# Optimization experiments

Measured on AMD Instinct MI355X. Metric: run time of the kernel, lower is better.

Reference implementation:

```python
import jax, jax.numpy as jnp
import numpy as np

EPS = 1e-7  # tf.keras.backend.epsilon()
DEGREE = 5
SCALE_BASE = 1.0
SCALE_LEGENDRE = 1.0


def legendre_basis(x, degree):
    # min/max normalization over the feature axis -> x_norm in [-1, 1]
    x_min = jnp.min(x, axis=-1, keepdims=True)
    x_max = jnp.max(x, axis=-1, keepdims=True)
    x_norm = 2.0 * (x - x_min) / (x_max - x_min + EPS) - 1.0
    polys = [jnp.ones_like(x_norm), x_norm]
    for n in range(2, degree + 1):
        p_n = ((2 * n - 1) * x_norm * polys[-1] - (n - 1) * polys[-2]) / n
        polys.append(p_n)
    return jnp.stack(polys, axis=-1)  # [b, i, degree+1]


def setup_inputs() -> dict:
    key = jax.random.key(0)
    k1, k2, k3 = jax.random.split(key, 3)
    b, i, o, d = 4096, 1024, 1024, DEGREE + 1
    x = jax.random.normal(k1, (b, i), dtype=jnp.float32)
    # HeUniform: limit = sqrt(6 / fan_in)
    lim_b = np.sqrt(6.0 / i)
    base_weight = jax.random.uniform(k2, (i, o), dtype=jnp.float32, minval=-lim_b, maxval=lim_b)
    legendre_weight = jax.random.uniform(k3, (i, o, d), dtype=jnp.float32, minval=-lim_b, maxval=lim_b)
    return {"x": x, "base_weight": base_weight, "legendre_weight": legendre_weight}


def reference(x, base_weight, legendre_weight):
    base_output = jax.nn.silu(x @ base_weight)  # [b, o]
    basis = legendre_basis(x, DEGREE)  # [b, i, d]
    # 'bi,iod,bid->bo' == fold x into the basis then contract (i, d)
    xb = x[..., None] * basis  # [b, i, d]
    legendre_output = jnp.einsum('bid,iod->bo', xb, legendre_weight)
    return SCALE_BASE * base_output + SCALE_LEGENDRE * legendre_output
```

## Files before the change

### kernel.cpp

```cpp
#include <hip/hip_runtime.h>
#include <stdint.h>

typedef unsigned short u16;
typedef unsigned int   u32;
typedef __attribute__((ext_vector_type(8))) short bhalf8;
typedef __attribute__((ext_vector_type(4))) float f32x4;

#define B_ROWS 4096
#define I_DIM  1024
#define O_DIM  1024
#define N_D    6
#define K_LEG  (I_DIM * N_D)

#define BM 256
#define BN 256
#define BK 32
#define NU 56
#define SLOT_BYTES 32768
#define LDS_BYTES  131072

__device__ __forceinline__ u16 f2b(float f) {
  u32 u = __float_as_uint(f);
  return (u16)((u + 0x7fffu + ((u >> 16) & 1u)) >> 16);
}

__device__ __forceinline__ void gld_lds16(const void* g, void* l) {
  __builtin_amdgcn_global_load_lds(
      (const __attribute__((address_space(1))) u32*)(uintptr_t)g,
      (__attribute__((address_space(3))) u32*)(u32)(uintptr_t)l, 16, 0, 0);
}

#define RS 201
__global__ void k_prep_w(const float* __restrict__ bw, const float* __restrict__ lw,
                         u16* __restrict__ Bb, u16* __restrict__ Bl) {
  __shared__ float t[32 * RS];
  if (blockIdx.x < 1024) {
    const int bx = blockIdx.x & 31, by = blockIdx.x >> 5;
    const int i0 = by * 32, o0 = bx * 32;
    const int c = threadIdx.x & 31, r0 = threadIdx.x >> 5;
    #pragma unroll
    for (int k = 0; k < 4; ++k) {
      int r = r0 + k * 8;
      t[r * 33 + c] = bw[(size_t)(i0 + r) * O_DIM + o0 + c];
    }
    __syncthreads();
    #pragma unroll
    for (int k = 0; k < 4; ++k) {
      int r = r0 + k * 8;
      Bb[(size_t)(o0 + r) * I_DIM + i0 + c] = f2b(t[c * 33 + r]);
    }
  } else {
    const int blk = blockIdx.x - 1024;
    const int bx = blk & 31, by = blk >> 5;
    const int i0 = by * 32, o0 = bx * 32;
    for (int q = threadIdx.x; q < 32 * 48; q += 256) {
      int ri = q / 48, s4 = q % 48;
      float4 v = *(const float4*)(lw + (size_t)(i0 + ri) * (O_DIM * N_D) + o0 * N_D + s4 * 4);
      float* p = t + ri * RS + s4 * 4;
      p[0] = v.x; p[1] = v.y; p[2] = v.z; p[3] = v.w;
    }
    __syncthreads();
    for (int q = threadIdx.x; q < 32 * 96; q += 256) {
      int ro = q / 96, k = q % 96;
      int e0 = 2 * k, e1 = 2 * k + 1;
      float v0 = t[(e0 / 6) * RS + ro * 6 + (e0 % 6)];
      float v1 = t[(e1 / 6) * RS + ro * 6 + (e1 % 6)];
      u32* dst = (u32*)(Bl + (size_t)(o0 + ro) * K_LEG + i0 * N_D);
      dst[k] = (u32)f2b(v0) | ((u32)f2b(v1) << 16);
    }
  }
}

__global__ void k_prep_basis(const float* __restrict__ x,
                             u16* __restrict__ Ab, u16* __restrict__ Al) {
  int b = blockIdx.x;
  int t = threadIdx.x;
  float4 v = ((const float4*)(x + (size_t)b * I_DIM))[t];
  float mn = fminf(fminf(v.x, v.y), fminf(v.z, v.w));
  float mx = fmaxf(fmaxf(v.x, v.y), fmaxf(v.z, v.w));
  #pragma unroll
  for (int off = 32; off > 0; off >>= 1) {
    mn = fminf(mn, __shfl_xor(mn, off, 64));
    mx = fmaxf(mx, __shfl_xor(mx, off, 64));
  }
  __shared__ float smn[4], smx[4];
  if ((t & 63) == 0) { smn[t >> 6] = mn; smx[t >> 6] = mx; }
  __syncthreads();
  mn = fminf(fminf(smn[0], smn[1]), fminf(smn[2], smn[3]));
  mx = fmaxf(fmaxf(smx[0], smx[1]), fmaxf(smx[2], smx[3]));
  float sc = 2.0f / (mx - mn + 1e-7f);

  float xs[4] = {v.x, v.y, v.z, v.w};
  u32 lb[12];
  #pragma unroll
  for (int e = 0; e < 4; ++e) {
    float xv = xs[e];
    float xn = (xv - mn) * sc - 1.0f;
    float p0 = 1.0f, p1 = xn;
    float p2 = (3.0f * xn * p1 - 1.0f * p0) * (1.0f / 2.0f);
    float p3 = (5.0f * xn * p2 - 2.0f * p1) * (1.0f / 3.0f);
    float p4 = (7.0f * xn * p3 - 3.0f * p2) * (1.0f / 4.0f);
    float p5 = (9.0f * xn * p4 - 4.0f * p3) * (1.0f / 5.0f);
    lb[e * 3 + 0] = (u32)f2b(xv * p0) | ((u32)f2b(xv * p1) << 16);
    lb[e * 3 + 1] = (u32)f2b(xv * p2) | ((u32)f2b(xv * p3) << 16);
    lb[e * 3 + 2] = (u32)f2b(xv * p4) | ((u32)f2b(xv * p5) << 16);
  }
  u32 a0 = (u32)f2b(xs[0]) | ((u32)f2b(xs[1]) << 16);
  u32 a1 = (u32)f2b(xs[2]) | ((u32)f2b(xs[3]) << 16);
  *(uint2*)(Ab + (size_t)b * I_DIM + t * 4) = make_uint2(a0, a1);
  uint4* dl = (uint4*)(Al + (size_t)b * K_LEG + t * 24);
  dl[0] = make_uint4(lb[0], lb[1], lb[2], lb[3]);
  dl[1] = make_uint4(lb[4], lb[5], lb[6], lb[7]);
  dl[2] = make_uint4(lb[8], lb[9], lb[10], lb[11]);
}

__global__ __launch_bounds__(512, 2) void k_gemm(
    const u16* __restrict__ Ab, const u16* __restrict__ Bb,
    const u16* __restrict__ Al, const u16* __restrict__ Bl,
    float* __restrict__ out, float* __restrict__ P) {
  extern __shared__ char lds[];

  const int tid  = threadIdx.x;
  const int wave = tid >> 6;
  const int lane = tid & 63;
  const int wm = wave >> 2;
  const int wn = wave & 3;
  const int rr = lane & 15;
  const int kg = lane >> 4;

  const int bid   = blockIdx.x;
  const int bx    = bid >> 4;
  const int by    = (bid >> 2) & 3;
  const int split = bid & 3;
  const size_t brow = (size_t)bx * BM;
  const size_t bcol = (size_t)by * BN;
  const bool s0 = (split == 0);
  const int legbase = s0 ? 0 : (24 + 56 * (split - 1));

  const int r4 = tid >> 2;
  const size_t cs = (size_t)((((tid & 3) ^ ((r4 >> 1) & 3))) * 8);
  char* const l0 = lds + (u32)wave * 1024;

  const u16 *gA0, *gA1, *gB0, *gB1;
  auto set_ptrs = [&](const u16* A, const u16* Bt, size_t ldk, size_t kt) {
    const size_t ko = kt * BK + cs;
    gA0 = A  + (brow + r4) * ldk + ko;
    gA1 = A  + (brow + 128 + r4) * ldk + ko;
    gB0 = Bt + (bcol + r4) * ldk + ko;
    gB1 = Bt + (bcol + 128 + r4) * ldk + ko;
  };
  if (s0) set_ptrs(Ab, Bb, I_DIM, 0);
  else    set_ptrs(Al, Bl, K_LEG, (size_t)legbase);

  const u32 axor  = (u32)((kg ^ ((rr >> 1) & 3)) * 16);
  const u32 abase = (u32)((wm * 128 + rr) * 64) + axor;
  const u32 bbase = 16384u + (u32)((wn * 64 + rr) * 64) + axor;

  f32x4 acc[8][4] = {};
  bhalf8 af_[4], af2_[4], bf_[4];

  #pragma unroll
  for (int v = 0; v < 3; ++v) {
    char* d = l0 + (size_t)v * SLOT_BYTES;
    gld_lds16(gA0, d);          gld_lds16(gA1, d + 8192);
    gld_lds16(gB0, d + 16384);  gld_lds16(gB1, d + 24576);
    gA0 += BK; gA1 += BK; gB0 += BK; gB1 += BK;
  }
  asm volatile("s_waitcnt vmcnt(8)" ::: "memory");
  __builtin_amdgcn_s_barrier();

#define PH0(u, DO_STAGE) do {                                                 \
    const char* p_ = lds + (size_t)((u) & 3) * SLOT_BYTES;                    \
    _Pragma("unroll")                                                         \
    for (int n = 0; n < 4; ++n) bf_[n] = *(const bhalf8*)(p_ + bbase + n * 1024); \
    _Pragma("unroll")                                                         \
    for (int m = 0; m < 4; ++m) af_[m] = *(const bhalf8*)(p_ + abase + m * 1024); \
    if (DO_STAGE) {                                                           \
      char* d_ = l0 + (size_t)(((u) + 3) & 3) * SLOT_BYTES;                   \
      gld_lds16(gA0, d_); gld_lds16(gA1, d_ + 8192);                          \
    }                                                                         \
    asm volatile("" ::: "memory");                                            \
    __builtin_amdgcn_s_barrier();                                             \
    asm volatile("s_waitcnt lgkmcnt(0)" ::: "memory");                        \
    __builtin_amdgcn_s_setprio(1);                                            \
    _Pragma("unroll")                                                         \
    for (int m = 0; m < 4; ++m)                                               \
      _Pragma("unroll")                                                       \
      for (int n = 0; n < 4; ++n)                                             \
        acc[m][n] = __builtin_amdgcn_mfma_f32_16x16x32_bf16(af_[m], bf_[n], acc[m][n], 0, 0, 0); \
    __builtin_amdgcn_s_setprio(0);                                            \
    __builtin_amdgcn_s_barrier();                                             \
  } while (0)

#define PH1(u, DO_STAGE, VM) do {                                             \
    const char* p_ = lds + (size_t)((u) & 3) * SLOT_BYTES;                    \
    _Pragma("unroll")                                                         \
    for (int m = 0; m < 4; ++m) af2_[m] = *(const bhalf8*)(p_ + abase + (4 + m) * 1024); \
    if (DO_STAGE) {                                                           \
      char* d_ = l0 + (size_t)(((u) + 3) & 3) * SLOT_BYTES;                   \
      gld_lds16(gB0, d_ + 16384); gld_lds16(gB1, d_ + 24576);                 \
      if (s0 && (u) + 4 == 32) set_ptrs(Al, Bl, K_LEG, 0);                    \
      else { gA0 += BK; gA1 += BK; gB0 += BK; gB1 += BK; }                    \
    }                                                                         \
    asm volatile("s_waitcnt vmcnt(" #VM ")" ::: "memory");                    \
    __builtin_amdgcn_s_barrier();                                             \
    asm volatile("s_waitcnt lgkmcnt(0)" ::: "memory");                        \
    __builtin_amdgcn_s_setprio(1);                                            \
    _Pragma("unroll")                                                         \
    for (int m = 0; m < 4; ++m)                                               \
      _Pragma("unroll")                                                       \
      for (int n = 0; n < 4; ++n)                                             \
        acc[4 + m][n] = __builtin_amdgcn_mfma_f32_16x16x32_bf16(af2_[m], bf_[n], acc[4 + m][n], 0, 0, 0); \
    __builtin_amdgcn_s_setprio(0);                                            \
    __builtin_amdgcn_s_barrier();                                             \
  } while (0)

  for (int u = 0; u < NU - 3; ++u) {
    if (s0 && u == 32) {
      #pragma unroll
      for (int m = 0; m < 8; ++m)
        #pragma unroll
        for (int n = 0; n < 4; ++n)
          #pragma unroll
          for (int j = 0; j < 4; ++j) {
            float v = acc[m][n][j];
            acc[m][n][j] = v / (1.0f + __expf(-v));
          }
    }
    PH0(u, true);
    PH1(u, true, 8);
  }
  PH0(53, false); PH1(53, false, 4);
  PH0(54, false); PH1(54, false, 0);
  PH0(55, false); PH1(55, false, 0);
#undef PH0
#undef PH1

  float* dst = s0 ? out : (P + (size_t)(split - 1) * ((size_t)B_ROWS * O_DIM));
  #pragma unroll
  for (int m = 0; m < 8; ++m)
    #pragma unroll
    for (int n = 0; n < 4; ++n) {
      const size_t r0 = brow + wm * 128 + m * 16 + kg * 4;
      const size_t c  = bcol + wn * 64 + n * 16 + rr;
      #pragma unroll
      for (int j = 0; j < 4; ++j)
        dst[(r0 + j) * O_DIM + c] = acc[m][n][j];
    }
}

__global__ void k_reduce(float* __restrict__ out, const float* __restrict__ P) {
  const size_t i = (size_t)blockIdx.x * 256 + threadIdx.x;
  const size_t NE = (size_t)B_ROWS * O_DIM / 4;
  float4 a = ((const float4*)out)[i];
  float4 b = ((const float4*)P)[i];
  float4 c = ((const float4*)P)[i + NE];
  float4 d = ((const float4*)P)[i + 2 * NE];
  a.x += b.x + c.x + d.x;  a.y += b.y + c.y + d.y;
  a.z += b.z + c.z + d.z;  a.w += b.w + c.w + d.w;
  ((float4*)out)[i] = a;
}

extern "C" void kernel_launch(void* const* d_in, const int* in_sizes, int n_in,
                              void* d_out, int out_size, void* d_ws, size_t ws_size,
                              hipStream_t stream) {
  const float* x  = (const float*)d_in[0];
  const float* bw = (const float*)d_in[1];
  const float* lw = (const float*)d_in[2];
  float* out = (float*)d_out;

  char* w = (char*)d_ws;
  u16*  Ab = (u16*)(w);
  u16*  Al = (u16*)(w + (size_t)8   * 1024 * 1024);
  u16*  Bb = (u16*)(w + (size_t)56  * 1024 * 1024);
  u16*  Bl = (u16*)(w + (size_t)58  * 1024 * 1024);
  float* P = (float*)(w + (size_t)72 * 1024 * 1024);

  hipFuncSetAttribute((const void*)k_gemm,
                      hipFuncAttributeMaxDynamicSharedMemorySize, LDS_BYTES);

  k_prep_w    <<<dim3(2048), 256, 0, stream>>>(bw, lw, Bb, Bl);
  k_prep_basis<<<dim3(B_ROWS), 256, 0, stream>>>(x, Ab, Al);
  k_gemm      <<<dim3(4 * (B_ROWS / BM) * (O_DIM / BN)), 512, LDS_BYTES, stream>>>(Ab, Bb, Al, Bl, out, P);
  k_reduce    <<<dim3((B_ROWS * O_DIM / 4) / 256), 256, 0, stream>>>(out, P);
}
```

Measured before the change: 112.8 us.

## Switch GEMM inner loop to 32x32x16 bf16 MFMA tiles with K-split phases

Replaces the 16x16x32 MFMA tiling with 32x32x16 MFMAs, so each wave now holds 4x2 accumulators of 16 floats. The two phases now split the BK=32 slice into two K halves over the full 128x64 wave tile, instead of splitting rows. This cuts the number of LDS fragment reads and MFMA issues per tile and uses the larger instruction's higher operand reuse. It also adds sched_barrier fences so the compiler cannot interleave the LDS reads with the MFMA block. The cost is a new LDS access pattern that may cause bank conflicts, and a changed accumulator-to-output mapping in the epilogue.

```diff
diff --git a/kernel.cpp b/kernel.cpp
--- a/kernel.cpp
+++ b/kernel.cpp
@@ -3,8 +3,8 @@
 
 typedef unsigned short u16;
 typedef unsigned int   u32;
-typedef __attribute__((ext_vector_type(8))) short bhalf8;
-typedef __attribute__((ext_vector_type(4))) float f32x4;
+typedef __attribute__((ext_vector_type(8)))  short bhalf8;
+typedef __attribute__((ext_vector_type(16))) float f32x16;
 
 #define B_ROWS 4096
 #define I_DIM  1024
@@ -125,8 +125,8 @@
   const int lane = tid & 63;
   const int wm = wave >> 2;
   const int wn = wave & 3;
-  const int rr = lane & 15;
-  const int kg = lane >> 4;
+  const u32 lr = lane & 31;
+  const u32 hi = (u32)lane >> 5;
 
   const int bid   = blockIdx.x;
   const int bx    = bid >> 4;
@@ -152,12 +152,14 @@
   if (s0) set_ptrs(Ab, Bb, I_DIM, 0);
   else    set_ptrs(Al, Bl, K_LEG, (size_t)legbase);
 
-  const u32 axor  = (u32)((kg ^ ((rr >> 1) & 3)) * 16);
-  const u32 abase = (u32)((wm * 128 + rr) * 64) + axor;
-  const u32 bbase = 16384u + (u32)((wn * 64 + rr) * 64) + axor;
-
-  f32x4 acc[8][4] = {};
-  bhalf8 af_[4], af2_[4], bf_[4];
+  const u32 sxor   = (lr >> 1) & 3;
+  const u32 chunk0 = ((0 + hi) ^ sxor) * 16;
+  const u32 chunk1 = ((2 + hi) ^ sxor) * 16;
+  const u32 abase_r = (u32)wm * 8192 + lr * 64;
+  const u32 bbase_r = 16384u + ((u32)wn >> 1) * 8192 + ((u32)wn & 1) * 4096 + lr * 64;
+
+  f32x16 acc[4][2] = {};
+  bhalf8 af_[4], bf_[2];
 
   #pragma unroll
   for (int v = 0; v < 3; ++v) {
@@ -172,9 +174,9 @@
 #define PH0(u, DO_STAGE) do {                                                 \
     const char* p_ = lds + (size_t)((u) & 3) * SLOT_BYTES;                    \
     _Pragma("unroll")                                                         \
-    for (int n = 0; n < 4; ++n) bf_[n] = *(const bhalf8*)(p_ + bbase + n * 1024); \
-    _Pragma("unroll")                                                         \
-    for (int m = 0; m < 4; ++m) af_[m] = *(const bhalf8*)(p_ + abase + m * 1024); \
+    for (int n = 0; n < 2; ++n) bf_[n] = *(const bhalf8*)(p_ + bbase_r + n * 2048 + chunk0); \
+    _Pragma("unroll")                                                         \
+    for (int m = 0; m < 4; ++m) af_[m] = *(const bhalf8*)(p_ + abase_r + m * 2048 + chunk0); \
     if (DO_STAGE) {                                                           \
       char* d_ = l0 + (size_t)(((u) + 3) & 3) * SLOT_BYTES;                   \
       gld_lds16(gA0, d_); gld_lds16(gA1, d_ + 8192);                          \
@@ -182,12 +184,13 @@
     asm volatile("" ::: "memory");                                            \
     __builtin_amdgcn_s_barrier();                                             \
     asm volatile("s_waitcnt lgkmcnt(0)" ::: "memory");                        \
+    __builtin_amdgcn_sched_barrier(0);                                        \
     __builtin_amdgcn_s_setprio(1);                                            \
     _Pragma("unroll")                                                         \
     for (int m = 0; m < 4; ++m)                                               \
       _Pragma("unroll")                                                       \
-      for (int n = 0; n < 4; ++n)                                             \
-        acc[m][n] = __builtin_amdgcn_mfma_f32_16x16x32_bf16(af_[m], bf_[n], acc[m][n], 0, 0, 0); \
+      for (int n = 0; n < 2; ++n)                                             \
+        acc[m][n] = __builtin_amdgcn_mfma_f32_32x32x16_bf16(af_[m], bf_[n], acc[m][n], 0, 0, 0); \
     __builtin_amdgcn_s_setprio(0);                                            \
     __builtin_amdgcn_s_barrier();                                             \
   } while (0)
@@ -195,7 +198,9 @@
 #define PH1(u, DO_STAGE, VM) do {                                             \
     const char* p_ = lds + (size_t)((u) & 3) * SLOT_BYTES;                    \
     _Pragma("unroll")                                                         \
-    for (int m = 0; m < 4; ++m) af2_[m] = *(const bhalf8*)(p_ + abase + (4 + m) * 1024); \
+    for (int n = 0; n < 2; ++n) bf_[n] = *(const bhalf8*)(p_ + bbase_r + n * 2048 + chunk1); \
+    _Pragma("unroll")                                                         \
+    for (int m = 0; m < 4; ++m) af_[m] = *(const bhalf8*)(p_ + abase_r + m * 2048 + chunk1); \
     if (DO_STAGE) {                                                           \
       char* d_ = l0 + (size_t)(((u) + 3) & 3) * SLOT_BYTES;                   \
       gld_lds16(gB0, d_ + 16384); gld_lds16(gB1, d_ + 24576);                 \
@@ -205,12 +210,13 @@
     asm volatile("s_waitcnt vmcnt(" #VM ")" ::: "memory");                    \
     __builtin_amdgcn_s_barrier();                                             \
     asm volatile("s_waitcnt lgkmcnt(0)" ::: "memory");                        \
+    __builtin_amdgcn_sched_barrier(0);                                        \
     __builtin_amdgcn_s_setprio(1);                                            \
     _Pragma("unroll")                                                         \
     for (int m = 0; m < 4; ++m)                                               \
       _Pragma("unroll")                                                       \
-      for (int n = 0; n < 4; ++n)                                             \
-        acc[4 + m][n] = __builtin_amdgcn_mfma_f32_16x16x32_bf16(af2_[m], bf_[n], acc[4 + m][n], 0, 0, 0); \
+      for (int n = 0; n < 2; ++n)                                             \
+        acc[m][n] = __builtin_amdgcn_mfma_f32_32x32x16_bf16(af_[m], bf_[n], acc[m][n], 0, 0, 0); \
     __builtin_amdgcn_s_setprio(0);                                            \
     __builtin_amdgcn_s_barrier();                                             \
   } while (0)
@@ -218,11 +224,11 @@
   for (int u = 0; u < NU - 3; ++u) {
     if (s0 && u == 32) {
       #pragma unroll
-      for (int m = 0; m < 8; ++m)
+      for (int m = 0; m < 4; ++m)
         #pragma unroll
-        for (int n = 0; n < 4; ++n)
+        for (int n = 0; n < 2; ++n)
           #pragma unroll
-          for (int j = 0; j < 4; ++j) {
+          for (int j = 0; j < 16; ++j) {
             float v = acc[m][n][j];
             acc[m][n][j] = v / (1.0f + __expf(-v));
           }
@@ -238,14 +244,16 @@
 
   float* dst = s0 ? out : (P + (size_t)(split - 1) * ((size_t)B_ROWS * O_DIM));
   #pragma unroll
-  for (int m = 0; m < 8; ++m)
+  for (int m = 0; m < 4; ++m)
     #pragma unroll
-    for (int n = 0; n < 4; ++n) {
-      const size_t r0 = brow + wm * 128 + m * 16 + kg * 4;
-      const size_t c  = bcol + wn * 64 + n * 16 + rr;
+    for (int n = 0; n < 2; ++n) {
+      const size_t rb = brow + wm * 128 + m * 32 + 4 * hi;
+      const size_t c  = bcol + wn * 64 + n * 32 + lr;
       #pragma unroll
-      for (int j = 0; j < 4; ++j)
-        dst[(r0 + j) * O_DIM + c] = acc[m][n][j];
+      for (int j = 0; j < 16; ++j) {
+        const size_t r = rb + (j & 3) + 8 * (j >> 2);
+        dst[r * O_DIM + c] = acc[m][n][j];
+      }
     }
 }
 
```

New measurement: 118.1 us. 1.05x slower.
